# Kernel optimization log

Measured on AMD Instinct MI355X. Metric: run time of the kernel, lower is better.

Reference implementation:

```python
import jax, jax.numpy as jnp
import numpy as np

D = 300      # GloVe embed size (hard-coded in module)
H = 150      # per-direction LSTM hidden (bi-output = 300 = hidden_size)
EPS = 1e-8   # torch F.cosine_similarity eps


def setup_inputs() -> dict:
    key = jax.random.key(0)
    ks = jax.random.split(key, 16)
    B, S, C, T = 256, 128, 256, 64
    n = lambda k, sh, sc=1.0: jax.random.normal(k, sh, dtype=jnp.float32) * sc
    return {
        "src_emb": n(ks[0], (B, S, D)),
        "col_emb": n(ks[1], (B, C, D)),
        "tab_emb": n(ks[2], (B, T, D)),
        "col_hot": (jax.random.uniform(ks[3], (B, C, 9)) < 0.3).astype(jnp.float32),
        "tab_hot": (jax.random.uniform(ks[4], (B, T, 5)) < 0.3).astype(jnp.float32),
        # BiLSTM params (gate order i,f,g,o)
        "Wx_f": n(ks[5], (D, 4 * H), 0.05), "Wh_f": n(ks[6], (H, 4 * H), 0.05), "b_f": jnp.zeros((4 * H,), jnp.float32),
        "Wx_b": n(ks[7], (D, 4 * H), 0.05), "Wh_b": n(ks[8], (H, 4 * H), 0.05), "b_b": jnp.zeros((4 * H,), jnp.float32),
        # type encoders (Linear 9->300, 5->300)
        "W_col": n(ks[9], (9, 2 * H), 0.1), "b_col": jnp.zeros((2 * H,), jnp.float32),
        "W_tab": n(ks[10], (5, 2 * H), 0.1), "b_tab": jnp.zeros((2 * H,), jnp.float32),
    }


def _lstm_dir(x_tbd, Wx, Wh, b, reverse):
    # x_tbd: [T, B, D] -> hs: [T, B, H], cT: [B, H]
    Bsz = x_tbd.shape[1]
    h0 = jnp.zeros((Bsz, H), x_tbd.dtype)
    def step(carry, xt):
        h, c = carry
        g = xt @ Wx + h @ Wh + b
        i, f, gg, o = jnp.split(g, 4, axis=-1)
        c = jax.nn.sigmoid(f) * c + jax.nn.sigmoid(i) * jnp.tanh(gg)
        h = jax.nn.sigmoid(o) * jnp.tanh(c)
        return (h, c), h
    (hT, cT), hs = jax.lax.scan(step, (h0, h0), x_tbd, reverse=reverse)
    return hs, cT


def _embed_context(src_enc, src_emb, cmp_emb):
    # cosine sim [B,C,S] then weighted sum of src_enc -> [B,C,2H]
    sn = jnp.maximum(jnp.linalg.norm(src_emb, axis=-1), EPS)   # [B,S]
    cn = jnp.maximum(jnp.linalg.norm(cmp_emb, axis=-1), EPS)   # [B,C]
    sim = jnp.einsum("bcd,bsd->bcs", cmp_emb, src_emb) / (cn[:, :, None] * sn[:, None, :])
    return jnp.einsum("bcs,bsd->bcd", sim, src_enc)


def reference(src_emb, col_emb, tab_emb, col_hot, tab_hot,
              Wx_f, Wh_f, b_f, Wx_b, Wh_b, b_b,
              W_col, b_col, W_tab, b_tab):
    x = jnp.transpose(src_emb, (1, 0, 2))               # [S,B,D]
    hs_f, c_f = _lstm_dir(x, Wx_f, Wh_f, b_f, False)
    hs_b, c_b = _lstm_dir(x, Wx_b, Wh_b, b_b, True)
    src_encoding = jnp.transpose(jnp.concatenate([hs_f, hs_b], -1), (1, 0, 2))  # [B,S,300]
    last_cell = jnp.concatenate([c_f, c_b], -1)          # [B,300]
    # dropout is identity in eval mode
    col_encoding = col_emb + _embed_context(src_encoding, src_emb, col_emb) + (col_hot @ W_col + b_col)
    tab_encoding = tab_emb + _embed_context(src_encoding, src_emb, tab_emb) + (tab_hot @ W_tab + b_tab)
    return src_encoding, col_encoding, tab_encoding, last_cell
```

## Files before the change

### kernel.cpp

```cpp
#include <hip/hip_runtime.h>
#include <math.h>

#define Bv 256
#define Sv 128
#define Cv 256
#define Tv 64
#define Dv 300
#define Hv 150
#define G4v 600

typedef _Float16 h8v __attribute__((ext_vector_type(8)));
typedef _Float16 h4v __attribute__((ext_vector_type(4)));
typedef float    f4v __attribute__((ext_vector_type(4)));

__global__ __launch_bounds__(256)
void row_norm_k(const float* __restrict__ x, int rows, float* __restrict__ out)
{
    int gtid = blockIdx.x * 256 + threadIdx.x;
    int wave = gtid >> 6;
    int lane = threadIdx.x & 63;
    if (wave >= rows) return;
    const float* row = x + (size_t)wave * Dv;
    float s = 0.f;
    for (int k = lane; k < Dv; k += 64) { float v = row[k]; s += v * v; }
    #pragma unroll
    for (int off = 32; off > 0; off >>= 1) s += __shfl_down(s, off, 64);
    if (lane == 0) out[wave] = fmaxf(sqrtf(s), 1e-8f);
}

__global__ __launch_bounds__(256)
void conv_a16_k(const float* __restrict__ A, _Float16* __restrict__ A16)
{
    int idx = blockIdx.x * 256 + threadIdx.x;
    int row = idx / 80;
    int k   = (idx - row * 80) * 4;
    float4 v = {0.f, 0.f, 0.f, 0.f};
    if (k < Dv) v = *(const float4*)&A[(size_t)row * Dv + k];
    h4v o;
    o[0] = (_Float16)v.x; o[1] = (_Float16)v.y;
    o[2] = (_Float16)v.z; o[3] = (_Float16)v.w;
    *(h4v*)&A16[(size_t)row * 320 + k] = o;
}

__global__ __launch_bounds__(320)
void conv_w16_k(const float* __restrict__ Wf, const float* __restrict__ Wb,
                _Float16* __restrict__ W16T)
{
    const int n   = blockIdx.x;
    const int dir = blockIdx.y;
    const int k   = threadIdx.x;
    const float* W = dir ? Wb : Wf;
    float v = (k < Dv && n < G4v) ? W[(size_t)k * G4v + n] : 0.f;
    W16T[((size_t)dir * 640 + n) * 320 + k] = (_Float16)v;
}

__global__ __launch_bounds__(256)
void gemm_xw_mfma_k(const _Float16* __restrict__ A16,
                    const _Float16* __restrict__ W16T,
                    const float* __restrict__ bf, const float* __restrict__ bb,
                    float* __restrict__ Gout)
{
    const int m0  = blockIdx.x * 128;
    const int n0  = blockIdx.y * 128;
    const int dir = blockIdx.z;
    const float* bias = dir ? bb : bf;
    const _Float16* Wd = W16T + (size_t)dir * 640 * 320;

    __shared__ _Float16 As[128][40];
    __shared__ _Float16 Bs[128][40];

    const int tid  = threadIdx.x;
    const int lane = tid & 63;
    const int w    = tid >> 6;
    const int wm   = w >> 1, wn = w & 1;
    const int r16  = lane & 15, q = lane >> 4;

    const int srow  = tid >> 1;
    const int sslot = (tid & 1) * 16;

    f4v acc[4][4];
    #pragma unroll
    for (int i = 0; i < 4; ++i)
        #pragma unroll
        for (int j = 0; j < 4; ++j) acc[i][j] = (f4v){0.f,0.f,0.f,0.f};

    for (int k0 = 0; k0 < 320; k0 += 32) {
        h8v av0 = *(const h8v*)&A16[(size_t)(m0 + srow) * 320 + k0 + sslot];
        h8v av1 = *(const h8v*)&A16[(size_t)(m0 + srow) * 320 + k0 + sslot + 8];
        h8v bv0 = *(const h8v*)&Wd [(size_t)(n0 + srow) * 320 + k0 + sslot];
        h8v bv1 = *(const h8v*)&Wd [(size_t)(n0 + srow) * 320 + k0 + sslot + 8];
        __syncthreads();
        *(h8v*)&As[srow][sslot]     = av0;
        *(h8v*)&As[srow][sslot + 8] = av1;
        *(h8v*)&Bs[srow][sslot]     = bv0;
        *(h8v*)&Bs[srow][sslot + 8] = bv1;
        __syncthreads();

        h8v af[4], bfr[4];
        #pragma unroll
        for (int mi = 0; mi < 4; ++mi)
            af[mi] = *(const h8v*)&As[wm*64 + mi*16 + r16][q*8];
        #pragma unroll
        for (int ni = 0; ni < 4; ++ni)
            bfr[ni] = *(const h8v*)&Bs[wn*64 + ni*16 + r16][q*8];
        #pragma unroll
        for (int mi = 0; mi < 4; ++mi)
            #pragma unroll
            for (int ni = 0; ni < 4; ++ni)
                acc[mi][ni] = __builtin_amdgcn_mfma_f32_16x16x32_f16(
                                  af[mi], bfr[ni], acc[mi][ni], 0, 0, 0);
    }

    #pragma unroll
    for (int ni = 0; ni < 4; ++ni) {
        int n = n0 + wn*64 + ni*16 + r16;
        if (n >= G4v) continue;
        float bn = bias[n];
        #pragma unroll
        for (int mi = 0; mi < 4; ++mi) {
            #pragma unroll
            for (int r = 0; r < 4; ++r) {
                int row = m0 + wm*64 + mi*16 + q*4 + r;
                int b   = row >> 7;
                int s   = row & 127;
                Gout[(((size_t)dir * Sv + s) * Bv + b) * G4v + n] = acc[mi][ni][r] + bn;
            }
        }
    }
}

__device__ __forceinline__ float sigm(float x) { return 1.0f / (1.0f + expf(-x)); }

__global__ __launch_bounds__(640, 1)
void lstm_mfma_k(const float* __restrict__ G,
                 const float* __restrict__ Wh_f, const float* __restrict__ Wh_b,
                 float* __restrict__ out_src,
                 float* __restrict__ out_cell)
{
    const int blk = blockIdx.x;
    const int dir = blk & 1;
    const int b0  = (blk >> 1) * 4;
    const float* Wh = dir ? Wh_b : Wh_f;
    const float* Gd = G + (size_t)dir * Sv * Bv * G4v;

    const int tid  = threadIdx.x;
    const int w    = tid >> 6;
    const int lane = tid & 63;
    const int q    = lane >> 4;
    const int cp   = lane & 15;
    const int hcol = w * 16 + cp;
    const bool colok = (hcol < Hv);

    __shared__ _Float16 h_sh[2][16][168];
    __shared__ float    g_sh[10][4][16][4];

    h8v Bf[4][5];
    #pragma unroll
    for (int g = 0; g < 4; ++g) {
        #pragma unroll
        for (int ks = 0; ks < 5; ++ks) {
            h8v v;
            #pragma unroll
            for (int j = 0; j < 8; ++j) {
                int k = 32*ks + 8*q + j;
                float x = (k < Hv && colok) ? Wh[(size_t)k * G4v + hcol + ((g*Hv))] : 0.f;
                v[j] = (_Float16)x;
            }
            Bf[g][ks] = v;
        }
    }

    for (int i = tid; i < 2*16*168; i += 640)
        ((_Float16*)h_sh)[i] = (_Float16)0.f;

    float c = 0.f;
    const int rp = q;

    float gc0, gc1, gc2, gc3;
    {
        int ss0 = dir ? (Sv - 1) : 0;
        const float* p = Gd + ((size_t)ss0 * Bv + b0 + rp) * G4v;
        gc0 = colok ? p[0*Hv + hcol] : 0.f;
        gc1 = colok ? p[1*Hv + hcol] : 0.f;
        gc2 = colok ? p[2*Hv + hcol] : 0.f;
        gc3 = colok ? p[3*Hv + hcol] : 0.f;
    }
    __syncthreads();

    int cur = 0;
    for (int s = 0; s < Sv; ++s) {
        const int ss = dir ? (Sv - 1 - s) : s;

        float gn0 = 0.f, gn1 = 0.f, gn2 = 0.f, gn3 = 0.f;
        if (s + 1 < Sv) {
            int ssn = dir ? (ss - 1) : (ss + 1);
            const float* p = Gd + ((size_t)ssn * Bv + b0 + rp) * G4v;
            if (colok) {
                gn0 = p[0*Hv + hcol]; gn1 = p[1*Hv + hcol];
                gn2 = p[2*Hv + hcol]; gn3 = p[3*Hv + hcol];
            }
        }

        f4v a0 = {0.f,0.f,0.f,0.f}, a1 = a0, a2 = a0, a3 = a0;
        #pragma unroll
        for (int ks = 0; ks < 5; ++ks) {
            h8v af = *(const h8v*)&h_sh[cur][cp][32*ks + 8*q];
            a0 = __builtin_amdgcn_mfma_f32_16x16x32_f16(af, Bf[0][ks], a0, 0, 0, 0);
            a1 = __builtin_amdgcn_mfma_f32_16x16x32_f16(af, Bf[1][ks], a1, 0, 0, 0);
            a2 = __builtin_amdgcn_mfma_f32_16x16x32_f16(af, Bf[2][ks], a2, 0, 0, 0);
            a3 = __builtin_amdgcn_mfma_f32_16x16x32_f16(af, Bf[3][ks], a3, 0, 0, 0);
        }

        if (q == 0) {
            *(f4v*)&g_sh[w][0][cp][0] = a0;
            *(f4v*)&g_sh[w][1][cp][0] = a1;
            *(f4v*)&g_sh[w][2][cp][0] = a2;
            *(f4v*)&g_sh[w][3][cp][0] = a3;
        }
        float gi = g_sh[w][0][cp][rp] + gc0;
        float gf = g_sh[w][1][cp][rp] + gc1;
        float gg = g_sh[w][2][cp][rp] + gc2;
        float go = g_sh[w][3][cp][rp] + gc3;

        float I  = sigm(gi);
        float F  = sigm(gf);
        float Gt = tanhf(gg);
        float O  = sigm(go);
        c = F * c + I * Gt;
        float h = O * tanhf(c);

        h_sh[cur ^ 1][rp][hcol] = (_Float16)h;
        if (colok)
            out_src[(((size_t)(b0 + rp)) * Sv + ss) * (2*Hv) + dir*Hv + hcol] = h;

        gc0 = gn0; gc1 = gn1; gc2 = gn2; gc3 = gn3;
        cur ^= 1;

        asm volatile("s_waitcnt lgkmcnt(0)" ::: "memory");
        __builtin_amdgcn_s_barrier();
        __builtin_amdgcn_sched_barrier(0);
    }

    if (colok)
        out_cell[(size_t)(b0 + rp) * (2*Hv) + dir*Hv + hcol] = c;
}

__global__ __launch_bounds__(256)
void trans_enc_k(const float* __restrict__ enc,
                 _Float16* __restrict__ hi, _Float16* __restrict__ lo)
{
    const int b  = blockIdx.z;
    const int s0 = blockIdx.x * 64;
    const int n0 = blockIdx.y * 64;
    __shared__ float t[64][65];
    const int tid = threadIdx.x;
    const int j  = tid & 63;
    const int i0 = (tid >> 6) * 16;
    #pragma unroll
    for (int ii = 0; ii < 16; ++ii) {
        int i = i0 + ii;
        int n = n0 + j;
        t[i][j] = (n < Dv) ? enc[((size_t)b*Sv + s0 + i)*Dv + n] : 0.f;
    }
    __syncthreads();
    #pragma unroll
    for (int ii = 0; ii < 16; ++ii) {
        int nr = i0 + ii;
        float v = t[j][nr];
        _Float16 hh = (_Float16)v;
        float l = v - (float)hh;
        size_t o = ((size_t)b*320 + n0 + nr)*128 + s0 + j;
        hi[o] = hh;
        lo[o] = (_Float16)l;
    }
}

__global__ __launch_bounds__(256)
void gemm_sim_mfma_k(const _Float16* __restrict__ cmp16,
                     const _Float16* __restrict__ src16,
                     const float* __restrict__ cn, const float* __restrict__ sn,
                     int M, _Float16* __restrict__ sim16)
{
    const int m0 = blockIdx.x * 128;
    const int b  = blockIdx.z;
    const _Float16* A  = cmp16 + (size_t)b * M * 320;
    const _Float16* Bm = src16 + (size_t)b * 128 * 320;

    __shared__ _Float16 As[128][40];
    __shared__ _Float16 Bs[128][40];

    const int tid  = threadIdx.x;
    const int lane = tid & 63;
    const int w    = tid >> 6;
    const int wm   = w >> 1, wn = w & 1;
    const int r16  = lane & 15, q = lane >> 4;

    const int srow  = tid >> 1;
    const int sslot = (tid & 1) * 16;
    const int arow  = (m0 + srow < M) ? (m0 + srow) : 0;

    f4v acc[4][4];
    #pragma unroll
    for (int i = 0; i < 4; ++i)
        #pragma unroll
        for (int j = 0; j < 4; ++j) acc[i][j] = (f4v){0.f,0.f,0.f,0.f};

    for (int k0 = 0; k0 < 320; k0 += 32) {
        h8v av0 = *(const h8v*)&A [(size_t)arow * 320 + k0 + sslot];
        h8v av1 = *(const h8v*)&A [(size_t)arow * 320 + k0 + sslot + 8];
        h8v bv0 = *(const h8v*)&Bm[(size_t)srow * 320 + k0 + sslot];
        h8v bv1 = *(const h8v*)&Bm[(size_t)srow * 320 + k0 + sslot + 8];
        __syncthreads();
        *(h8v*)&As[srow][sslot]     = av0;
        *(h8v*)&As[srow][sslot + 8] = av1;
        *(h8v*)&Bs[srow][sslot]     = bv0;
        *(h8v*)&Bs[srow][sslot + 8] = bv1;
        __syncthreads();

        h8v af[4], bfr[4];
        #pragma unroll
        for (int mi = 0; mi < 4; ++mi)
            af[mi] = *(const h8v*)&As[wm*64 + mi*16 + r16][q*8];
        #pragma unroll
        for (int ni = 0; ni < 4; ++ni)
            bfr[ni] = *(const h8v*)&Bs[wn*64 + ni*16 + r16][q*8];
        #pragma unroll
        for (int mi = 0; mi < 4; ++mi)
            #pragma unroll
            for (int ni = 0; ni < 4; ++ni)
                acc[mi][ni] = __builtin_amdgcn_mfma_f32_16x16x32_f16(
                                  af[mi], bfr[ni], acc[mi][ni], 0, 0, 0);
    }

    #pragma unroll
    for (int ni = 0; ni < 4; ++ni) {
        int s = wn*64 + ni*16 + r16;
        float snv = sn[(size_t)b * 128 + s];
        #pragma unroll
        for (int mi = 0; mi < 4; ++mi) {
            #pragma unroll
            for (int r = 0; r < 4; ++r) {
                int m = m0 + wm*64 + mi*16 + q*4 + r;
                if (m < M) {
                    float v = acc[mi][ni][r] / (cn[(size_t)b * M + m] * snv);
                    sim16[((size_t)b * M + m) * 128 + s] = (_Float16)v;
                }
            }
        }
    }
}

__global__ __launch_bounds__(256, 2)
void gemm_ctx_fused_k(const _Float16* __restrict__ sim16,
                      const _Float16* __restrict__ encHi,
                      const _Float16* __restrict__ encLo,
                      const float* __restrict__ emb,
                      const float* __restrict__ hot,
                      const float* __restrict__ W,
                      const float* __restrict__ bias,
                      int M, int hd, float* __restrict__ outp)
{
    const int b  = blockIdx.z;
    const int m0 = blockIdx.x * 64;
    const int tid = threadIdx.x;
    const int lane = tid & 63;
    const int w = tid >> 6;
    const int q = lane >> 4, cp = lane & 15;

    __shared__ _Float16 As[64][136];
    __shared__ float Wsh[9*304];
    __shared__ float bsh[304];
    __shared__ float hotsh[64*9];

    {
        const int srow = tid >> 2;
        const int scol = (tid & 3) * 32;
        const _Float16* src = sim16 + ((size_t)b * M + m0 + srow) * 128 + scol;
        *(h8v*)&As[srow][scol]      = *(const h8v*)&src[0];
        *(h8v*)&As[srow][scol + 8]  = *(const h8v*)&src[8];
        *(h8v*)&As[srow][scol + 16] = *(const h8v*)&src[16];
        *(h8v*)&As[srow][scol + 24] = *(const h8v*)&src[24];
    }
    for (int i = tid; i < hd*304; i += 256) {
        int jj = i / 304, nn = i - jj*304;
        Wsh[i] = (nn < Dv) ? W[(size_t)jj * Dv + nn] : 0.f;
    }
    for (int i = tid; i < 304; i += 256) bsh[i] = (i < Dv) ? bias[i] : 0.f;
    for (int i = tid; i < 64*hd; i += 256) hotsh[i] = hot[((size_t)b * M + m0) * hd + i];
    __syncthreads();

    h8v af[4][4];
    #pragma unroll
    for (int mi = 0; mi < 4; ++mi)
        #pragma unroll
        for (int ks = 0; ks < 4; ++ks)
            af[mi][ks] = *(const h8v*)&As[mi*16 + cp][32*ks + 8*q];

    f4v acc[4][5];
    #pragma unroll
    for (int mi = 0; mi < 4; ++mi)
        #pragma unroll
        for (int nt = 0; nt < 5; ++nt) acc[mi][nt] = (f4v){0.f,0.f,0.f,0.f};

    const int nbase = w * 80;
    #pragma unroll
    for (int pass = 0; pass < 2; ++pass) {
        const _Float16* encp = pass ? encLo : encHi;
        #pragma unroll
        for (int nt = 0; nt < 5; ++nt) {
            int n = nbase + nt*16 + cp;
            const _Float16* bp = encp + ((size_t)b * 320 + n) * 128 + 8*q;
            h8v b0 = *(const h8v*)&bp[0];
            h8v b1 = *(const h8v*)&bp[32];
            h8v b2 = *(const h8v*)&bp[64];
            h8v b3 = *(const h8v*)&bp[96];
            #pragma unroll
            for (int mi = 0; mi < 4; ++mi) {
                acc[mi][nt] = __builtin_amdgcn_mfma_f32_16x16x32_f16(af[mi][0], b0, acc[mi][nt], 0, 0, 0);
                acc[mi][nt] = __builtin_amdgcn_mfma_f32_16x16x32_f16(af[mi][1], b1, acc[mi][nt], 0, 0, 0);
                acc[mi][nt] = __builtin_amdgcn_mfma_f32_16x16x32_f16(af[mi][2], b2, acc[mi][nt], 0, 0, 0);
                acc[mi][nt] = __builtin_amdgcn_mfma_f32_16x16x32_f16(af[mi][3], b3, acc[mi][nt], 0, 0, 0);
            }
        }
    }

    #pragma unroll
    for (int nt = 0; nt < 5; ++nt) {
        int n = nbase + nt*16 + cp;
        if (n >= Dv) continue;
        float bn = bsh[n];
        #pragma unroll
        for (int mi = 0; mi < 4; ++mi) {
            #pragma unroll
            for (int r = 0; r < 4; ++r) {
                int ml = mi*16 + 4*q + r;
                int m  = m0 + ml;
                float v = acc[mi][nt][r] + bn + emb[((size_t)b * M + m) * Dv + n];
                for (int jj = 0; jj < hd; ++jj)
                    v = fmaf(hotsh[ml*hd + jj], Wsh[jj*304 + n], v);
                outp[((size_t)b * M + m) * Dv + n] = v;
            }
        }
    }
}

extern "C" void kernel_launch(void* const* d_in, const int* in_sizes, int n_in,
                              void* d_out, int out_size, void* d_ws, size_t ws_size,
                              hipStream_t stream)
{
    (void)in_sizes; (void)n_in; (void)out_size; (void)ws_size;
    const float* src_emb = (const float*)d_in[0];
    const float* col_emb = (const float*)d_in[1];
    const float* tab_emb = (const float*)d_in[2];
    const float* col_hot = (const float*)d_in[3];
    const float* tab_hot = (const float*)d_in[4];
    const float* Wx_f = (const float*)d_in[5];
    const float* Wh_f = (const float*)d_in[6];
    const float* b_f  = (const float*)d_in[7];
    const float* Wx_b = (const float*)d_in[8];
    const float* Wh_b = (const float*)d_in[9];
    const float* b_b  = (const float*)d_in[10];
    const float* W_col = (const float*)d_in[11];
    const float* b_col = (const float*)d_in[12];
    const float* W_tab = (const float*)d_in[13];
    const float* b_tab = (const float*)d_in[14];

    float* out      = (float*)d_out;
    float* out_src  = out;
    float* out_col  = out + 9830400;
    float* out_tab  = out + 29491200;
    float* out_cell = out + 34406400;

    float* ws = (float*)d_ws;
    float* Gbuf = ws;
    _Float16* encHi    = (_Float16*)(ws);
    _Float16* encLo    = (_Float16*)(ws + 5242880);
    _Float16* sim16_col= (_Float16*)(ws + 11000000);
    _Float16* sim16_tab= (_Float16*)(ws + 16000000);
    float* sn = ws + 39321600;
    float* cn = sn + 32768;
    float* tn = cn + 65536;

    _Float16* A16   = (_Float16*)(out + 9830400);
    _Float16* W16T  = A16 + (size_t)32768 * 320;
    _Float16* col16 = (_Float16*)(out + 15278080);
    _Float16* tab16 = (_Float16*)(out + 29491200);

    conv_a16_k<<<32768*80/256, 256, 0, stream>>>(src_emb, A16);
    conv_a16_k<<<65536*80/256, 256, 0, stream>>>(col_emb, col16);
    conv_a16_k<<<16384*80/256, 256, 0, stream>>>(tab_emb, tab16);
    conv_w16_k<<<dim3(640, 2), 320, 0, stream>>>(Wx_f, Wx_b, W16T);

    row_norm_k<<<32768/4, 256, 0, stream>>>(src_emb, 32768, sn);
    row_norm_k<<<65536/4, 256, 0, stream>>>(col_emb, 65536, cn);
    row_norm_k<<<16384/4, 256, 0, stream>>>(tab_emb, 16384, tn);

    gemm_xw_mfma_k<<<dim3(256, 5, 2), 256, 0, stream>>>(A16, W16T, b_f, b_b, Gbuf);

    lstm_mfma_k<<<128, 640, 0, stream>>>(Gbuf, Wh_f, Wh_b, out_src, out_cell);

    trans_enc_k<<<dim3(2, 5, 256), 256, 0, stream>>>(out_src, encHi, encLo);

    gemm_sim_mfma_k<<<dim3(2, 1, 256), 256, 0, stream>>>(col16, A16, cn, sn, 256, sim16_col);
    gemm_sim_mfma_k<<<dim3(1, 1, 256), 256, 0, stream>>>(tab16, A16, tn, sn, 64,  sim16_tab);

    gemm_ctx_fused_k<<<dim3(4, 1, 256), 256, 0, stream>>>(
        sim16_col, encHi, encLo, col_emb, col_hot, W_col, b_col, 256, 9, out_col);
    gemm_ctx_fused_k<<<dim3(1, 1, 256), 256, 0, stream>>>(
        sim16_tab, encHi, encLo, tab_emb, tab_hot, W_tab, b_tab, 64, 5, out_tab);
}
```

Baseline: 688.4 us.

## Restructure LSTM recurrence to 16 batches per block with transposed MFMA

Swaps MFMA operands so the recurrent weights are the A operand and the hidden states the B operand. Each block now handles 16 batch rows instead of 4, which fills all 16 MFMA columns that previously carried mostly zero-padded rows. Gate accumulators are read straight from registers, with no shared-memory round trip. The precomputed input gates seed the accumulator, and sigmoid and tanh use fast exp/rcp intrinsics. The grid shrinks from 128 to 32 blocks, so many CUs sit idle during the serial recurrence, and the fast intrinsics slightly reduce accuracy.

New measurement: 781.1 us. 13.5% more time.

```diff
diff --git a/kernel.cpp b/kernel.cpp
--- a/kernel.cpp
+++ b/kernel.cpp
@@ -12,6 +12,7 @@
 typedef _Float16 h8v __attribute__((ext_vector_type(8)));
 typedef _Float16 h4v __attribute__((ext_vector_type(4)));
 typedef float    f4v __attribute__((ext_vector_type(4)));
+typedef float    f2v __attribute__((ext_vector_type(2)));
 
 __global__ __launch_bounds__(256)
 void row_norm_k(const float* __restrict__ x, int rows, float* __restrict__ out)
@@ -129,7 +130,16 @@
     }
 }
 
-__device__ __forceinline__ float sigm(float x) { return 1.0f / (1.0f + expf(-x)); }
+__device__ __forceinline__ float sigm_f(float x)
+{
+    return __builtin_amdgcn_rcpf(1.f + __expf(-x));
+}
+__device__ __forceinline__ float tanh_f(float x)
+{
+    float e = __expf(-2.f * __builtin_fabsf(x));
+    float r = (1.f - e) * __builtin_amdgcn_rcpf(1.f + e);
+    return __builtin_copysignf(r, x);
+}
 
 __global__ __launch_bounds__(640, 1)
 void lstm_mfma_k(const float* __restrict__ G,
@@ -139,7 +149,7 @@
 {
     const int blk = blockIdx.x;
     const int dir = blk & 1;
-    const int b0  = (blk >> 1) * 4;
+    const int b0  = (blk >> 1) * 16;
     const float* Wh = dir ? Wh_b : Wh_f;
     const float* Gd = G + (size_t)dir * Sv * Bv * G4v;
 
@@ -148,13 +158,13 @@
     const int lane = tid & 63;
     const int q    = lane >> 4;
     const int cp   = lane & 15;
-    const int hcol = w * 16 + cp;
-    const bool colok = (hcol < Hv);
+    const int nb   = w * 16 + 4 * q;
+    const int ncol = w * 16 + cp;
+    const int batch = b0 + cp;
 
     __shared__ _Float16 h_sh[2][16][168];
-    __shared__ float    g_sh[10][4][16][4];
-
-    h8v Bf[4][5];
+
+    h8v Af[4][5];
     #pragma unroll
     for (int g = 0; g < 4; ++g) {
         #pragma unroll
@@ -163,27 +173,30 @@
             #pragma unroll
             for (int j = 0; j < 8; ++j) {
                 int k = 32*ks + 8*q + j;
-                float x = (k < Hv && colok) ? Wh[(size_t)k * G4v + hcol + ((g*Hv))] : 0.f;
+                float x = (k < Hv && ncol < Hv)
+                        ? Wh[(size_t)k * G4v + g*Hv + ncol] : 0.f;
                 v[j] = (_Float16)x;
             }
-            Bf[g][ks] = v;
+            Af[g][ks] = v;
         }
     }
 
     for (int i = tid; i < 2*16*168; i += 640)
         ((_Float16*)h_sh)[i] = (_Float16)0.f;
 
-    float c = 0.f;
-    const int rp = q;
-
-    float gc0, gc1, gc2, gc3;
+    float cst[4] = {0.f, 0.f, 0.f, 0.f};
+
+    f4v gc[4];
     {
         int ss0 = dir ? (Sv - 1) : 0;
-        const float* p = Gd + ((size_t)ss0 * Bv + b0 + rp) * G4v;
-        gc0 = colok ? p[0*Hv + hcol] : 0.f;
-        gc1 = colok ? p[1*Hv + hcol] : 0.f;
-        gc2 = colok ? p[2*Hv + hcol] : 0.f;
-        gc3 = colok ? p[3*Hv + hcol] : 0.f;
+        const float* gp = Gd + ((size_t)ss0 * Bv + batch) * G4v + nb;
+        #pragma unroll
+        for (int g = 0; g < 4; ++g) {
+            const float* p = gp + g*Hv;
+            f2v lo = (nb     < Hv) ? *(const f2v*)p       : (f2v){0.f,0.f};
+            f2v hi = (nb + 2 < Hv) ? *(const f2v*)(p + 2) : (f2v){0.f,0.f};
+            gc[g] = (f4v){lo[0], lo[1], hi[0], hi[1]};
+        }
     }
     __syncthreads();
 
@@ -191,49 +204,55 @@
     for (int s = 0; s < Sv; ++s) {
         const int ss = dir ? (Sv - 1 - s) : s;
 
-        float gn0 = 0.f, gn1 = 0.f, gn2 = 0.f, gn3 = 0.f;
+        f4v gn[4];
+        #pragma unroll
+        for (int g = 0; g < 4; ++g) gn[g] = (f4v){0.f,0.f,0.f,0.f};
         if (s + 1 < Sv) {
             int ssn = dir ? (ss - 1) : (ss + 1);
-            const float* p = Gd + ((size_t)ssn * Bv + b0 + rp) * G4v;
-            if (colok) {
-                gn0 = p[0*Hv + hcol]; gn1 = p[1*Hv + hcol];
-                gn2 = p[2*Hv + hcol]; gn3 = p[3*Hv + hcol];
+            const float* gp = Gd + ((size_t)ssn * Bv + batch) * G4v + nb;
+            #pragma unroll
+            for (int g = 0; g < 4; ++g) {
+                const float* p = gp + g*Hv;
+                f2v lo = (nb     < Hv) ? *(const f2v*)p       : (f2v){0.f,0.f};
+                f2v hi = (nb + 2 < Hv) ? *(const f2v*)(p + 2) : (f2v){0.f,0.f};
+                gn[g] = (f4v){lo[0], lo[1], hi[0], hi[1]};
             }
         }
 
-        f4v a0 = {0.f,0.f,0.f,0.f}, a1 = a0, a2 = a0, a3 = a0;
+        f4v a0 = gc[0], a1 = gc[1], a2 = gc[2], a3 = gc[3];
         #pragma unroll
         for (int ks = 0; ks < 5; ++ks) {
-            h8v af = *(const h8v*)&h_sh[cur][cp][32*ks + 8*q];
-            a0 = __builtin_amdgcn_mfma_f32_16x16x32_f16(af, Bf[0][ks], a0, 0, 0, 0);
-            a1 = __builtin_amdgcn_mfma_f32_16x16x32_f16(af, Bf[1][ks], a1, 0, 0, 0);
-            a2 = __builtin_amdgcn_mfma_f32_16x16x32_f16(af, Bf[2][ks], a2, 0, 0, 0);
-            a3 = __builtin_amdgcn_mfma_f32_16x16x32_f16(af, Bf[3][ks], a3, 0, 0, 0);
-        }
-
-        if (q == 0) {
-            *(f4v*)&g_sh[w][0][cp][0] = a0;
-            *(f4v*)&g_sh[w][1][cp][0] = a1;
-            *(f4v*)&g_sh[w][2][cp][0] = a2;
-            *(f4v*)&g_sh[w][3][cp][0] = a3;
-        }
-        float gi = g_sh[w][0][cp][rp] + gc0;
-        float gf = g_sh[w][1][cp][rp] + gc1;
-        float gg = g_sh[w][2][cp][rp] + gc2;
-        float go = g_sh[w][3][cp][rp] + gc3;
-
-        float I  = sigm(gi);
-        float F  = sigm(gf);
-        float Gt = tanhf(gg);
-        float O  = sigm(go);
-        c = F * c + I * Gt;
-        float h = O * tanhf(c);
-
-        h_sh[cur ^ 1][rp][hcol] = (_Float16)h;
-        if (colok)
-            out_src[(((size_t)(b0 + rp)) * Sv + ss) * (2*Hv) + dir*Hv + hcol] = h;
-
-        gc0 = gn0; gc1 = gn1; gc2 = gn2; gc3 = gn3;
+            h8v bf = *(const h8v*)&h_sh[cur][cp][32*ks + 8*q];
+            a0 = __builtin_amdgcn_mfma_f32_16x16x32_f16(Af[0][ks], bf, a0, 0, 0, 0);
+            a1 = __builtin_amdgcn_mfma_f32_16x16x32_f16(Af[1][ks], bf, a1, 0, 0, 0);
+            a2 = __builtin_amdgcn_mfma_f32_16x16x32_f16(Af[2][ks], bf, a2, 0, 0, 0);
+            a3 = __builtin_amdgcn_mfma_f32_16x16x32_f16(Af[3][ks], bf, a3, 0, 0, 0);
+        }
+
+        float hv[4];
+        #pragma unroll
+        for (int r = 0; r < 4; ++r) {
+            float I  = sigm_f(a0[r]);
+            float F  = sigm_f(a1[r]);
+            float Gt = tanh_f(a2[r]);
+            float O  = sigm_f(a3[r]);
+            cst[r] = F * cst[r] + I * Gt;
+            float h = O * tanh_f(cst[r]);
+            hv[r] = (nb + r < Hv) ? h : 0.f;
+        }
+
+        h4v hp;
+        hp[0] = (_Float16)hv[0]; hp[1] = (_Float16)hv[1];
+        hp[2] = (_Float16)hv[2]; hp[3] = (_Float16)hv[3];
+        *(h4v*)&h_sh[cur ^ 1][cp][nb] = hp;
+
+        {
+            float* op = out_src + ((size_t)batch * Sv + ss) * (2*Hv) + dir*Hv + nb;
+            if (nb < Hv)     *(f2v*)op       = (f2v){hv[0], hv[1]};
+            if (nb + 2 < Hv) *(f2v*)(op + 2) = (f2v){hv[2], hv[3]};
+        }
+
+        gc[0] = gn[0]; gc[1] = gn[1]; gc[2] = gn[2]; gc[3] = gn[3];
         cur ^= 1;
 
         asm volatile("s_waitcnt lgkmcnt(0)" ::: "memory");
@@ -241,8 +260,11 @@
         __builtin_amdgcn_sched_barrier(0);
     }
 
-    if (colok)
-        out_cell[(size_t)(b0 + rp) * (2*Hv) + dir*Hv + hcol] = c;
+    {
+        float* op = out_cell + (size_t)batch * (2*Hv) + dir*Hv + nb;
+        if (nb < Hv)     *(f2v*)op       = (f2v){cst[0], cst[1]};
+        if (nb + 2 < Hv) *(f2v*)(op + 2) = (f2v){cst[2], cst[3]};
+    }
 }
 
 __global__ __launch_bounds__(256)
@@ -497,7 +519,7 @@
 
     gemm_xw_mfma_k<<<dim3(256, 5, 2), 256, 0, stream>>>(A16, W16T, b_f, b_b, Gbuf);
 
-    lstm_mfma_k<<<128, 640, 0, stream>>>(Gbuf, Wh_f, Wh_b, out_src, out_cell);
+    lstm_mfma_k<<<32, 640, 0, stream>>>(Gbuf, Wh_f, Wh_b, out_src, out_cell);
 
     trans_enc_k<<<dim3(2, 5, 256), 256, 0, stream>>>(out_src, encHi, encLo);
 
```

## Store LSTM input gates in fp16, prefetch two steps ahead, use fast activations

Applied to the files above, without the earlier changes.

The input-projection GEMM now writes its gate preactivations as fp16 instead of fp32, which halves the size of the large intermediate buffer and the bytes the recurrent LSTM kernel reads each step. The LSTM kernel prefetches gate inputs two timesteps ahead instead of one, to hide global load latency in the serial loop. Sigmoid and tanh are replaced by __expf/rcp-based approximations to shorten the per-step critical path. Both the fp16 storage and the approximate activations reduce precision, and that error can build up over the 128-step recurrence.

New measurement: 623.8 us. 1.1x faster.

```diff
diff --git a/kernel.cpp b/kernel.cpp
--- a/kernel.cpp
+++ b/kernel.cpp
@@ -12,6 +12,7 @@
 typedef _Float16 h8v __attribute__((ext_vector_type(8)));
 typedef _Float16 h4v __attribute__((ext_vector_type(4)));
 typedef float    f4v __attribute__((ext_vector_type(4)));
+typedef float    f2v __attribute__((ext_vector_type(2)));
 
 __global__ __launch_bounds__(256)
 void row_norm_k(const float* __restrict__ x, int rows, float* __restrict__ out)
@@ -58,7 +59,7 @@
 void gemm_xw_mfma_k(const _Float16* __restrict__ A16,
                     const _Float16* __restrict__ W16T,
                     const float* __restrict__ bf, const float* __restrict__ bb,
-                    float* __restrict__ Gout)
+                    _Float16* __restrict__ Gout)
 {
     const int m0  = blockIdx.x * 128;
     const int n0  = blockIdx.y * 128;
@@ -123,16 +124,26 @@
                 int row = m0 + wm*64 + mi*16 + q*4 + r;
                 int b   = row >> 7;
                 int s   = row & 127;
-                Gout[(((size_t)dir * Sv + s) * Bv + b) * G4v + n] = acc[mi][ni][r] + bn;
+                Gout[(((size_t)dir * Sv + s) * Bv + b) * G4v + n] =
+                    (_Float16)(acc[mi][ni][r] + bn);
             }
         }
     }
 }
 
-__device__ __forceinline__ float sigm(float x) { return 1.0f / (1.0f + expf(-x)); }
+__device__ __forceinline__ float sigm_f(float x)
+{
+    return __builtin_amdgcn_rcpf(1.f + __expf(-x));
+}
+__device__ __forceinline__ float tanh_f(float x)
+{
+    float e = __expf(-2.f * __builtin_fabsf(x));
+    float r = (1.f - e) * __builtin_amdgcn_rcpf(1.f + e);
+    return __builtin_copysignf(r, x);
+}
 
 __global__ __launch_bounds__(640, 1)
-void lstm_mfma_k(const float* __restrict__ G,
+void lstm_mfma_k(const _Float16* __restrict__ G16,
                  const float* __restrict__ Wh_f, const float* __restrict__ Wh_b,
                  float* __restrict__ out_src,
                  float* __restrict__ out_cell)
@@ -141,7 +152,7 @@
     const int dir = blk & 1;
     const int b0  = (blk >> 1) * 4;
     const float* Wh = dir ? Wh_b : Wh_f;
-    const float* Gd = G + (size_t)dir * Sv * Bv * G4v;
+    const _Float16* Gd = G16 + (size_t)dir * Sv * Bv * G4v;
 
     const int tid  = threadIdx.x;
     const int w    = tid >> 6;
@@ -150,6 +161,8 @@
     const int cp   = lane & 15;
     const int hcol = w * 16 + cp;
     const bool colok = (hcol < Hv);
+    const int hc   = colok ? hcol : 0;
+    const int rp   = q;
 
     __shared__ _Float16 h_sh[2][16][168];
     __shared__ float    g_sh[10][4][16][4];
@@ -163,7 +176,7 @@
             #pragma unroll
             for (int j = 0; j < 8; ++j) {
                 int k = 32*ks + 8*q + j;
-                float x = (k < Hv && colok) ? Wh[(size_t)k * G4v + hcol + ((g*Hv))] : 0.f;
+                float x = (k < Hv && colok) ? Wh[(size_t)k * G4v + g*Hv + hcol] : 0.f;
                 v[j] = (_Float16)x;
             }
             Bf[g][ks] = v;
@@ -174,16 +187,18 @@
         ((_Float16*)h_sh)[i] = (_Float16)0.f;
 
     float c = 0.f;
-    const int rp = q;
-
-    float gc0, gc1, gc2, gc3;
+
+    _Float16 gA[4], gB[4];
     {
         int ss0 = dir ? (Sv - 1) : 0;
-        const float* p = Gd + ((size_t)ss0 * Bv + b0 + rp) * G4v;
-        gc0 = colok ? p[0*Hv + hcol] : 0.f;
-        gc1 = colok ? p[1*Hv + hcol] : 0.f;
-        gc2 = colok ? p[2*Hv + hcol] : 0.f;
-        gc3 = colok ? p[3*Hv + hcol] : 0.f;
+        int ss1 = dir ? (Sv - 2) : 1;
+        const _Float16* p0 = Gd + ((size_t)ss0 * Bv + b0 + rp) * G4v;
+        const _Float16* p1 = Gd + ((size_t)ss1 * Bv + b0 + rp) * G4v;
+        #pragma unroll
+        for (int g = 0; g < 4; ++g) {
+            gA[g] = p0[g*Hv + hc];
+            gB[g] = p1[g*Hv + hc];
+        }
     }
     __syncthreads();
 
@@ -191,14 +206,14 @@
     for (int s = 0; s < Sv; ++s) {
         const int ss = dir ? (Sv - 1 - s) : s;
 
-        float gn0 = 0.f, gn1 = 0.f, gn2 = 0.f, gn3 = 0.f;
-        if (s + 1 < Sv) {
-            int ssn = dir ? (ss - 1) : (ss + 1);
-            const float* p = Gd + ((size_t)ssn * Bv + b0 + rp) * G4v;
-            if (colok) {
-                gn0 = p[0*Hv + hcol]; gn1 = p[1*Hv + hcol];
-                gn2 = p[2*Hv + hcol]; gn3 = p[3*Hv + hcol];
-            }
+        _Float16 gC[4];
+        #pragma unroll
+        for (int g = 0; g < 4; ++g) gC[g] = (_Float16)0.f;
+        if (s + 2 < Sv) {
+            int ss2 = dir ? (ss - 2) : (ss + 2);
+            const _Float16* p = Gd + ((size_t)ss2 * Bv + b0 + rp) * G4v;
+            #pragma unroll
+            for (int g = 0; g < 4; ++g) gC[g] = p[g*Hv + hc];
         }
 
         f4v a0 = {0.f,0.f,0.f,0.f}, a1 = a0, a2 = a0, a3 = a0;
@@ -217,23 +232,24 @@
             *(f4v*)&g_sh[w][2][cp][0] = a2;
             *(f4v*)&g_sh[w][3][cp][0] = a3;
         }
-        float gi = g_sh[w][0][cp][rp] + gc0;
-        float gf = g_sh[w][1][cp][rp] + gc1;
-        float gg = g_sh[w][2][cp][rp] + gc2;
-        float go = g_sh[w][3][cp][rp] + gc3;
-
-        float I  = sigm(gi);
-        float F  = sigm(gf);
-        float Gt = tanhf(gg);
-        float O  = sigm(go);
+        float gi = g_sh[w][0][cp][rp] + (float)gA[0];
+        float gf = g_sh[w][1][cp][rp] + (float)gA[1];
+        float gg = g_sh[w][2][cp][rp] + (float)gA[2];
+        float go = g_sh[w][3][cp][rp] + (float)gA[3];
+
+        float I  = sigm_f(gi);
+        float F  = sigm_f(gf);
+        float Gt = tanh_f(gg);
+        float O  = sigm_f(go);
         c = F * c + I * Gt;
-        float h = O * tanhf(c);
+        float h = O * tanh_f(c);
 
         h_sh[cur ^ 1][rp][hcol] = (_Float16)h;
         if (colok)
             out_src[(((size_t)(b0 + rp)) * Sv + ss) * (2*Hv) + dir*Hv + hcol] = h;
 
-        gc0 = gn0; gc1 = gn1; gc2 = gn2; gc3 = gn3;
+        #pragma unroll
+        for (int g = 0; g < 4; ++g) { gA[g] = gB[g]; gB[g] = gC[g]; }
         cur ^= 1;
 
         asm volatile("s_waitcnt lgkmcnt(0)" ::: "memory");
@@ -472,7 +488,7 @@
     float* out_cell = out + 34406400;
 
     float* ws = (float*)d_ws;
-    float* Gbuf = ws;
+    _Float16* Gbuf16 = (_Float16*)ws;
     _Float16* encHi    = (_Float16*)(ws);
     _Float16* encLo    = (_Float16*)(ws + 5242880);
     _Float16* sim16_col= (_Float16*)(ws + 11000000);
@@ -495,9 +511,9 @@
     row_norm_k<<<65536/4, 256, 0, stream>>>(col_emb, 65536, cn);
     row_norm_k<<<16384/4, 256, 0, stream>>>(tab_emb, 16384, tn);
 
-    gemm_xw_mfma_k<<<dim3(256, 5, 2), 256, 0, stream>>>(A16, W16T, b_f, b_b, Gbuf);
-
-    lstm_mfma_k<<<128, 640, 0, stream>>>(Gbuf, Wh_f, Wh_b, out_src, out_cell);
+    gemm_xw_mfma_k<<<dim3(256, 5, 2), 256, 0, stream>>>(A16, W16T, b_f, b_b, Gbuf16);
+
+    lstm_mfma_k<<<128, 640, 0, stream>>>(Gbuf16, Wh_f, Wh_b, out_src, out_cell);
 
     trans_enc_k<<<dim3(2, 5, 256), 256, 0, stream>>>(out_src, encHi, encLo);
 
```
